# Kernel optimization log

Measured on AMD Instinct MI355X. Metric: run time of the kernel, lower is better.

The kernel has to match this reference:

```python
import jax, jax.numpy as jnp
import numpy as np

S, B, D, H = 2048, 2, 1024, 16
DK = D // H  # 64

def setup_inputs() -> dict:
    key0 = jax.random.key(0)
    ks = jax.random.split(key0, 11)
    scale = 0.02
    inp = {
        'query': jax.random.normal(ks[0], (S, B, D), jnp.float32),
        'key':   jax.random.normal(ks[1], (S, B, D), jnp.float32),
        'value': jax.random.normal(ks[2], (S, B, D), jnp.float32),
        # nn.Linear weights stored torch-style [out_features, in_features]
        'Wq': jax.random.normal(ks[3], (H * DK, D), jnp.float32) * scale,
        'bq': jnp.zeros((H * DK,), jnp.float32),
        'Wk': jax.random.normal(ks[4], (H * DK, D), jnp.float32) * scale,
        'bk': jnp.zeros((H * DK,), jnp.float32),
        'Wv': jax.random.normal(ks[5], (H * DK, D), jnp.float32) * scale,
        'bv': jnp.zeros((H * DK,), jnp.float32),
        'Wo': jax.random.normal(ks[6], (D, D), jnp.float32) * scale,
        'bo': jnp.zeros((D,), jnp.float32),
    }
    return inp

def _proj(x, W, b):
    # x: [S,B,D] -> [S,B,H,DK]
    y = jnp.einsum('sbd,ed->sbe', x, W) + b
    return y.reshape(x.shape[0], x.shape[1], H, DK)

def reference(query, key, value, Wq, bq, Wk, bk, Wv, bv, Wo, bo):
    q = _proj(query, Wq, bq)   # [S,B,H,DK]
    k = _proj(key,   Wk, bk)
    v = _proj(value, Wv, bv)
    # NOTE: original forward never applies self.scale -> unscaled QK^T (faithful)
    scores = jnp.einsum('ibhd,jbhd->ijbh', q, k)      # [Sq,Sk,B,H]
    attn = jax.nn.softmax(scores, axis=1)             # softmax over key axis j
    x = jnp.einsum('ijbh,jbhd->ibhd', attn, v)        # [S,B,H,DK]
    x = x.reshape(q.shape[0], q.shape[1], H * DK)     # [S,B,D]
    out = jnp.einsum('sbd,ed->sbe', x, Wo) + bo       # [S,B,D]
    return out
```

## Files before the change

### kernel.cpp

```cpp
#include <hip/hip_runtime.h>
#include <stdint.h>

#define S_LEN  2048
#define BATCH  2
#define DMODEL 1024
#define NHEAD  16
#define DKH    64

typedef __attribute__((ext_vector_type(8))) __bf16 bf16x8;
typedef __attribute__((ext_vector_type(4))) float  f32x4;
typedef unsigned short u16;
typedef unsigned int   u32;

#if __has_builtin(__builtin_amdgcn_exp2f)
#define EXP2(x) __builtin_amdgcn_exp2f(x)
#else
#define EXP2(x) __expf(0.69314718055994531f * (x))
#endif

__device__ __forceinline__ u16 f2bf(float f) {
  union { float f; u32 u; } v; v.f = f;
  u32 r = v.u + 0x7fffu + ((v.u >> 16) & 1u);
  return (u16)(r >> 16);
}

__global__ void cvt3_kernel(const float4* __restrict__ a, const float4* __restrict__ b,
                            const float4* __restrict__ c,
                            ushort4* __restrict__ oa, ushort4* __restrict__ ob,
                            ushort4* __restrict__ oc, int n4) {
  int i = blockIdx.x * blockDim.x + threadIdx.x;
  if (i >= n4) return;
  const float4* src = (blockIdx.y == 0) ? a : (blockIdx.y == 1) ? b : c;
  ushort4*      dst = (blockIdx.y == 0) ? oa : (blockIdx.y == 1) ? ob : oc;
  float4 v = src[i];
  ushort4 o;
  o.x = f2bf(v.x); o.y = f2bf(v.y); o.z = f2bf(v.z); o.w = f2bf(v.w);
  dst[i] = o;
}

__global__ void cvt4_kernel(const float4* __restrict__ a, const float4* __restrict__ b,
                            const float4* __restrict__ c, const float4* __restrict__ d,
                            ushort4* __restrict__ oa, ushort4* __restrict__ ob,
                            ushort4* __restrict__ oc, ushort4* __restrict__ od, int n4) {
  int i = blockIdx.x * blockDim.x + threadIdx.x;
  if (i >= n4) return;
  const float4* src = (blockIdx.y == 0) ? a : (blockIdx.y == 1) ? b : (blockIdx.y == 2) ? c : d;
  ushort4*      dst = (blockIdx.y == 0) ? oa : (blockIdx.y == 1) ? ob : (blockIdx.y == 2) ? oc : od;
  float4 v = src[i];
  ushort4 o;
  o.x = f2bf(v.x); o.y = f2bf(v.y); o.z = f2bf(v.z); o.w = f2bf(v.w);
  dst[i] = o;
}

__global__ __launch_bounds__(256, 2)
void gemm_qkv(const u16* __restrict__ Abase, const u16* __restrict__ Wbase,
              const float* __restrict__ b0, const float* __restrict__ b1,
              const float* __restrict__ b2, u16* __restrict__ Obase) {
  __shared__ __align__(16) u16 As[128 * 32];
  __shared__ __align__(16) u16 Bs[128 * 32];

  const int z = blockIdx.z;
  const u16* A = Abase + (size_t)z * (S_LEN * BATCH * DMODEL);
  const u16* W = Wbase + (size_t)z * (DMODEL * DMODEL);
  const float* bias = (z == 0) ? b0 : (z == 1) ? b1 : b2;
  u16* O = Obase + (size_t)z * (S_LEN * BATCH * DMODEL);
  const float scl = (z == 0) ? 1.4426950408889634f : 1.0f;

  const int tid  = threadIdx.x;
  const int wave = tid >> 6, lane = tid & 63;
  const int quad = lane >> 4, lcol = lane & 15;
  const int m0 = blockIdx.y * 128, n0 = blockIdx.x * 128;
  const int wm = (wave >> 1) * 64, wn = (wave & 1) * 64;

  f32x4 acc[4][4] = {};

  for (int k0 = 0; k0 < DMODEL; k0 += 32) {
#pragma unroll
    for (int r = 0; r < 2; ++r) {
      int idx = r * 256 + tid;
      int row = idx >> 2, col = (idx & 3) * 8;
      const u16* gA = A + (size_t)(m0 + row) * DMODEL + k0 + col;
      const u16* gW = W + (size_t)(n0 + row) * DMODEL + k0 + col;
      u16* lA = As + (size_t)(r * 256 + (tid & 192)) * 8;
      u16* lB = Bs + (size_t)(r * 256 + (tid & 192)) * 8;
      __builtin_amdgcn_global_load_lds((const __attribute__((address_space(1))) void*)gA,
                                       (__attribute__((address_space(3))) void*)lA, 16, 0, 0);
      __builtin_amdgcn_global_load_lds((const __attribute__((address_space(1))) void*)gW,
                                       (__attribute__((address_space(3))) void*)lB, 16, 0, 0);
    }
    __syncthreads();

    const u16* aBase = As + (wm + lcol) * 32 + quad * 8;
    const u16* bBase = Bs + (wn + lcol) * 32 + quad * 8;
    bf16x8 af[4], bfr[4];
#pragma unroll
    for (int i = 0; i < 4; ++i) af[i]  = *(const bf16x8*)(aBase + i * 16 * 32);
#pragma unroll
    for (int j = 0; j < 4; ++j) bfr[j] = *(const bf16x8*)(bBase + j * 16 * 32);
#pragma unroll
    for (int i = 0; i < 4; ++i)
#pragma unroll
      for (int j = 0; j < 4; ++j)
        acc[i][j] = __builtin_amdgcn_mfma_f32_16x16x32_bf16(af[i], bfr[j], acc[i][j], 0, 0, 0);
    __syncthreads();
  }

#pragma unroll
  for (int i = 0; i < 4; ++i) {
#pragma unroll
    for (int j = 0; j < 4; ++j) {
      int n = n0 + wn + j * 16 + lcol;
      int h = n >> 6, dk = n & 63;
      float bv = bias[n];
#pragma unroll
      for (int r = 0; r < 4; ++r) {
        int m = m0 + wm + i * 16 + quad * 4 + r;
        int s = m >> 1, b = m & 1;
        O[((size_t)(b * NHEAD + h) * S_LEN + s) * DKH + dk] = f2bf((acc[i][j][r] + bv) * scl);
      }
    }
  }
}

__global__ __launch_bounds__(256, 2)
void gemm_o(const u16* __restrict__ A, const u16* __restrict__ W,
            const float* __restrict__ bias, float* __restrict__ O) {
  __shared__ __align__(16) u16 As[128 * 32];
  __shared__ __align__(16) u16 Bs[64 * 32];

  const int tid  = threadIdx.x;
  const int wave = tid >> 6, lane = tid & 63;
  const int quad = lane >> 4, lcol = lane & 15;
  const int m0 = blockIdx.y * 128, n0 = blockIdx.x * 64;
  const int wm = (wave >> 1) * 64, wn = (wave & 1) * 32;

  f32x4 acc[4][2] = {};

  for (int k0 = 0; k0 < DMODEL; k0 += 32) {
#pragma unroll
    for (int r = 0; r < 2; ++r) {
      int idx = r * 256 + tid;
      int row = idx >> 2, col = (idx & 3) * 8;
      const u16* gA = A + (size_t)(m0 + row) * DMODEL + k0 + col;
      u16* lA = As + (size_t)(r * 256 + (tid & 192)) * 8;
      __builtin_amdgcn_global_load_lds((const __attribute__((address_space(1))) void*)gA,
                                       (__attribute__((address_space(3))) void*)lA, 16, 0, 0);
    }
    {
      int row = tid >> 2, col = (tid & 3) * 8;
      const u16* gW = W + (size_t)(n0 + row) * DMODEL + k0 + col;
      u16* lB = Bs + (size_t)(tid & 192) * 8;
      __builtin_amdgcn_global_load_lds((const __attribute__((address_space(1))) void*)gW,
                                       (__attribute__((address_space(3))) void*)lB, 16, 0, 0);
    }
    __syncthreads();

    const u16* aBase = As + (wm + lcol) * 32 + quad * 8;
    const u16* bBase = Bs + (wn + lcol) * 32 + quad * 8;
    bf16x8 af[4], bfr[2];
#pragma unroll
    for (int i = 0; i < 4; ++i) af[i]  = *(const bf16x8*)(aBase + i * 16 * 32);
#pragma unroll
    for (int j = 0; j < 2; ++j) bfr[j] = *(const bf16x8*)(bBase + j * 16 * 32);
#pragma unroll
    for (int i = 0; i < 4; ++i)
#pragma unroll
      for (int j = 0; j < 2; ++j)
        acc[i][j] = __builtin_amdgcn_mfma_f32_16x16x32_bf16(af[i], bfr[j], acc[i][j], 0, 0, 0);
    __syncthreads();
  }

#pragma unroll
  for (int i = 0; i < 4; ++i) {
#pragma unroll
    for (int j = 0; j < 2; ++j) {
      int n = n0 + wn + j * 16 + lcol;
      float bv = bias[n];
#pragma unroll
      for (int r = 0; r < 4; ++r) {
        int m = m0 + wm + i * 16 + quad * 4 + r;
        O[(size_t)m * DMODEL + n] = acc[i][j][r] + bv;
      }
    }
  }
}

__global__ __launch_bounds__(256, 2)
void attn_kernel(const u16* __restrict__ Q, const u16* __restrict__ K,
                 const u16* __restrict__ V, u16* __restrict__ O) {
  __shared__ __align__(16) u16 Ks[2][64 * 72];
  __shared__ __align__(16) u16 Vts[2][64 * 72];
  __shared__ __align__(16) u16 Ps[4][32 * 72];
  __shared__ float l_s[128];

  const int tid  = threadIdx.x;
  const int wave = tid >> 6, lane = tid & 63;
  const int quad = lane >> 4, lcol = lane & 15;
  const int bh = blockIdx.y;
  const int q0 = blockIdx.x * 128;

  const size_t headOff = (size_t)bh * S_LEN * DKH;
  const u16* Qg = Q + headOff;
  const u16* Kg = K + headOff;
  const u16* Vg = V + headOff;

  bf16x8 qf[2][2];
#pragma unroll
  for (int s = 0; s < 2; ++s)
#pragma unroll
    for (int ks = 0; ks < 2; ++ks)
      qf[s][ks] = *(const bf16x8*)(Qg + (size_t)(q0 + wave * 32 + s * 16 + lcol) * DKH +
                                   ks * 32 + quad * 8);

  const int vkp  = tid & 31;
  const int vo   = tid >> 5;
  const int krow = tid >> 3, kc0 = (tid & 7) * 8;

  {
    uint4 k0 = *(const uint4*)(Kg + (size_t)krow * DKH + kc0);
    uint4 k1 = *(const uint4*)(Kg + (size_t)(32 + krow) * DKH + kc0);
    const u16* vp = Vg + (size_t)(2 * vkp) * DKH + 8 * vo;
    uint4 a = *(const uint4*)vp;
    uint4 b = *(const uint4*)(vp + DKH);
    *(uint4*)(Ks[0] + krow * 72 + kc0)        = k0;
    *(uint4*)(Ks[0] + (32 + krow) * 72 + kc0) = k1;
#pragma unroll
    for (int w = 0; w < 4; ++w) {
      u32 aw = ((const u32*)&a)[w], bw = ((const u32*)&b)[w];
      *(u32*)(Vts[0] + (size_t)(8 * vo + 2 * w) * 72 + 2 * vkp)     = __builtin_amdgcn_perm(bw, aw, 0x05040100u);
      *(u32*)(Vts[0] + (size_t)(8 * vo + 2 * w + 1) * 72 + 2 * vkp) = __builtin_amdgcn_perm(bw, aw, 0x07060302u);
    }
  }

  f32x4 o_acc[2][4] = {};
  float lsum[2] = {0.f, 0.f};

  for (int it = 0; it < S_LEN / 64; ++it) {
    const int cur = it & 1;
    const int ktn = (it + 1) * 64;
    const bool has = (ktn < S_LEN);

    uint4 nk0, nk1, nva, nvb;
    if (has) {
      nk0 = *(const uint4*)(Kg + (size_t)(ktn + krow) * DKH + kc0);
      nk1 = *(const uint4*)(Kg + (size_t)(ktn + 32 + krow) * DKH + kc0);
      const u16* vp = Vg + (size_t)(ktn + 2 * vkp) * DKH + 8 * vo;
      nva = *(const uint4*)vp;
      nvb = *(const uint4*)(vp + DKH);
    }
    __syncthreads();

    const u16* ksrc = Ks[cur];
    const u16* vsrc = Vts[cur];

    f32x4 sc[2][4] = {};
#pragma unroll
    for (int ks = 0; ks < 2; ++ks) {
      bf16x8 ak[4];
#pragma unroll
      for (int j = 0; j < 4; ++j)
        ak[j] = *(const bf16x8*)(ksrc + (j * 16 + lcol) * 72 + ks * 32 + quad * 8);
      __builtin_amdgcn_s_setprio(1);
#pragma unroll
      for (int s = 0; s < 2; ++s)
#pragma unroll
        for (int j = 0; j < 4; ++j)
          sc[s][j] = __builtin_amdgcn_mfma_f32_16x16x32_bf16(ak[j], qf[s][ks], sc[s][j], 0, 0, 0);
      __builtin_amdgcn_s_setprio(0);
    }

#pragma unroll
    for (int s = 0; s < 2; ++s) {
      u16* prow = Ps[wave] + (s * 16 + lcol) * 72;
#pragma unroll
      for (int j = 0; j < 4; ++j) {
        float p0 = EXP2(sc[s][j][0]);
        float p1 = EXP2(sc[s][j][1]);
        float p2 = EXP2(sc[s][j][2]);
        float p3 = EXP2(sc[s][j][3]);
        lsum[s] += (p0 + p1) + (p2 + p3);
        u32 w0, w1;
        asm("v_cvt_pk_bf16_f32 %0, %1, %2" : "=v"(w0) : "v"(p0), "v"(p1));
        asm("v_cvt_pk_bf16_f32 %0, %1, %2" : "=v"(w1) : "v"(p2), "v"(p3));
        uint2 pk; pk.x = w0; pk.y = w1;
        *(uint2*)(prow + j * 16 + quad * 4) = pk;
      }
    }

#pragma unroll
    for (int ks = 0; ks < 2; ++ks) {
      bf16x8 bv[4];
#pragma unroll
      for (int jd = 0; jd < 4; ++jd)
        bv[jd] = *(const bf16x8*)(vsrc + (jd * 16 + lcol) * 72 + ks * 32 + quad * 8);
      __builtin_amdgcn_s_setprio(1);
#pragma unroll
      for (int s = 0; s < 2; ++s) {
        bf16x8 ap = *(const bf16x8*)(Ps[wave] + (s * 16 + lcol) * 72 + ks * 32 + quad * 8);
#pragma unroll
        for (int jd = 0; jd < 4; ++jd)
          o_acc[s][jd] = __builtin_amdgcn_mfma_f32_16x16x32_bf16(ap, bv[jd], o_acc[s][jd], 0, 0, 0);
      }
      __builtin_amdgcn_s_setprio(0);
    }

    if (has) {
      u16* kdst = Ks[cur ^ 1];
      u16* vdst = Vts[cur ^ 1];
      *(uint4*)(kdst + krow * 72 + kc0)        = nk0;
      *(uint4*)(kdst + (32 + krow) * 72 + kc0) = nk1;
#pragma unroll
      for (int w = 0; w < 4; ++w) {
        u32 aw = ((const u32*)&nva)[w], bw = ((const u32*)&nvb)[w];
        *(u32*)(vdst + (size_t)(8 * vo + 2 * w) * 72 + 2 * vkp)     = __builtin_amdgcn_perm(bw, aw, 0x05040100u);
        *(u32*)(vdst + (size_t)(8 * vo + 2 * w + 1) * 72 + 2 * vkp) = __builtin_amdgcn_perm(bw, aw, 0x07060302u);
      }
    }
  }

#pragma unroll
  for (int s = 0; s < 2; ++s) {
    lsum[s] += __shfl_xor(lsum[s], 16);
    lsum[s] += __shfl_xor(lsum[s], 32);
  }
  if (lane < 16) {
    l_s[wave * 32 + lane]      = lsum[0];
    l_s[wave * 32 + 16 + lane] = lsum[1];
  }
  __syncthreads();

  const int b = bh >> 4, h = bh & 15;
#pragma unroll
  for (int s = 0; s < 2; ++s) {
#pragma unroll
    for (int r = 0; r < 4; ++r) {
      float inv = 1.f / l_s[wave * 32 + s * 16 + quad * 4 + r];
      int sq = q0 + wave * 32 + s * 16 + quad * 4 + r;
#pragma unroll
      for (int jd = 0; jd < 4; ++jd) {
        int dk = jd * 16 + lcol;
        O[((size_t)(sq * BATCH + b)) * DMODEL + h * DKH + dk] = f2bf(o_acc[s][jd][r] * inv);
      }
    }
  }
}

extern "C" void kernel_launch(void* const* d_in, const int* in_sizes, int n_in,
                              void* d_out, int out_size, void* d_ws, size_t ws_size,
                              hipStream_t stream) {
  const float* q  = (const float*)d_in[0];
  const float* k  = (const float*)d_in[1];
  const float* v  = (const float*)d_in[2];
  const float* Wq = (const float*)d_in[3];
  const float* bq = (const float*)d_in[4];
  const float* Wk = (const float*)d_in[5];
  const float* bk = (const float*)d_in[6];
  const float* Wv = (const float*)d_in[7];
  const float* bv = (const float*)d_in[8];
  const float* Wo = (const float*)d_in[9];
  const float* bo = (const float*)d_in[10];

  const int NX = S_LEN * BATCH * DMODEL;
  const int NW = DMODEL * DMODEL;

  u16* ws  = (u16*)d_ws;
  u16* Xq  = ws;
  u16* Wqb = Xq  + 3 * (size_t)NX;
  u16* Qb  = Wqb + 4 * (size_t)NW;
  u16* Xo  = Qb  + 3 * (size_t)NX;

  u16* Xk  = Xq + NX, *Xv = Xq + 2 * (size_t)NX;
  u16* Wkb = Wqb + NW, *Wvb = Wqb + 2 * (size_t)NW, *Wob = Wqb + 3 * (size_t)NW;
  u16* Kb  = Qb + NX, *Vb = Qb + 2 * (size_t)NX;

  dim3 g3(NX / 4 / 256, 3);
  cvt3_kernel<<<g3, 256, 0, stream>>>((const float4*)q, (const float4*)k, (const float4*)v,
                                      (ushort4*)Xq, (ushort4*)Xk, (ushort4*)Xv, NX / 4);
  dim3 g4(NW / 4 / 256, 4);
  cvt4_kernel<<<g4, 256, 0, stream>>>((const float4*)Wq, (const float4*)Wk, (const float4*)Wv,
                                      (const float4*)Wo,
                                      (ushort4*)Wqb, (ushort4*)Wkb, (ushort4*)Wvb, (ushort4*)Wob,
                                      NW / 4);

  dim3 gqkv(DMODEL / 128, (S_LEN * BATCH) / 128, 3);
  gemm_qkv<<<gqkv, 256, 0, stream>>>(Xq, Wqb, bq, bk, bv, Qb);

  dim3 ga(S_LEN / 128, BATCH * NHEAD);
  attn_kernel<<<ga, 256, 0, stream>>>(Qb, Kb, Vb, Xo);

  dim3 go(DMODEL / 64, (S_LEN * BATCH) / 128);
  gemm_o<<<go, 256, 0, stream>>>(Xo, Wob, bo, (float*)d_out);
}
```

Measured before the change: 226.1 us.

## Use 8 waves per attention block with 16 query rows each

The attention kernel now launches 512 threads, giving each wave 16 query rows instead of 32. This halves per-wave accumulator and score registers and raises wave-level parallelism. K and V tile staging is split so half the waves load K and half load and transpose V. The row-sum exchange through shared memory and its extra barrier are replaced by a lane shuffle. In exchange, each K/V tile read from LDS is now shared across more waves, so LDS read traffic per MFMA doubles.

```diff
diff --git a/kernel.cpp b/kernel.cpp
--- a/kernel.cpp
+++ b/kernel.cpp
@@ -185,13 +185,12 @@
   }
 }
 
-__global__ __launch_bounds__(256, 2)
+__global__ __launch_bounds__(512, 4)
 void attn_kernel(const u16* __restrict__ Q, const u16* __restrict__ K,
                  const u16* __restrict__ V, u16* __restrict__ O) {
   __shared__ __align__(16) u16 Ks[2][64 * 72];
   __shared__ __align__(16) u16 Vts[2][64 * 72];
-  __shared__ __align__(16) u16 Ps[4][32 * 72];
-  __shared__ float l_s[128];
+  __shared__ __align__(16) u16 Ps[8][16 * 72];
 
   const int tid  = threadIdx.x;
   const int wave = tid >> 6, lane = tid & 63;
@@ -204,26 +203,26 @@
   const u16* Kg = K + headOff;
   const u16* Vg = V + headOff;
 
-  bf16x8 qf[2][2];
-#pragma unroll
-  for (int s = 0; s < 2; ++s)
-#pragma unroll
-    for (int ks = 0; ks < 2; ++ks)
-      qf[s][ks] = *(const bf16x8*)(Qg + (size_t)(q0 + wave * 32 + s * 16 + lcol) * DKH +
-                                   ks * 32 + quad * 8);
-
-  const int vkp  = tid & 31;
-  const int vo   = tid >> 5;
-  const int krow = tid >> 3, kc0 = (tid & 7) * 8;
-
-  {
+  bf16x8 qf[2];
+#pragma unroll
+  for (int ks = 0; ks < 2; ++ks)
+    qf[ks] = *(const bf16x8*)(Qg + (size_t)(q0 + wave * 16 + lcol) * DKH + ks * 32 + quad * 8);
+
+  const int t4   = tid & 255;
+  const int krow = t4 >> 3, kc0 = (t4 & 7) * 8;
+  const int vkp  = t4 & 31;
+  const int vo   = t4 >> 5;
+  const bool isK = (wave < 4);
+
+  if (isK) {
     uint4 k0 = *(const uint4*)(Kg + (size_t)krow * DKH + kc0);
     uint4 k1 = *(const uint4*)(Kg + (size_t)(32 + krow) * DKH + kc0);
+    *(uint4*)(Ks[0] + krow * 72 + kc0)        = k0;
+    *(uint4*)(Ks[0] + (32 + krow) * 72 + kc0) = k1;
+  } else {
     const u16* vp = Vg + (size_t)(2 * vkp) * DKH + 8 * vo;
     uint4 a = *(const uint4*)vp;
     uint4 b = *(const uint4*)(vp + DKH);
-    *(uint4*)(Ks[0] + krow * 72 + kc0)        = k0;
-    *(uint4*)(Ks[0] + (32 + krow) * 72 + kc0) = k1;
 #pragma unroll
     for (int w = 0; w < 4; ++w) {
       u32 aw = ((const u32*)&a)[w], bw = ((const u32*)&b)[w];
@@ -232,28 +231,31 @@
     }
   }
 
-  f32x4 o_acc[2][4] = {};
-  float lsum[2] = {0.f, 0.f};
+  f32x4 o_acc[4] = {};
+  float lsum = 0.f;
 
   for (int it = 0; it < S_LEN / 64; ++it) {
     const int cur = it & 1;
     const int ktn = (it + 1) * 64;
     const bool has = (ktn < S_LEN);
 
-    uint4 nk0, nk1, nva, nvb;
+    uint4 n0, n1;
     if (has) {
-      nk0 = *(const uint4*)(Kg + (size_t)(ktn + krow) * DKH + kc0);
-      nk1 = *(const uint4*)(Kg + (size_t)(ktn + 32 + krow) * DKH + kc0);
-      const u16* vp = Vg + (size_t)(ktn + 2 * vkp) * DKH + 8 * vo;
-      nva = *(const uint4*)vp;
-      nvb = *(const uint4*)(vp + DKH);
+      if (isK) {
+        n0 = *(const uint4*)(Kg + (size_t)(ktn + krow) * DKH + kc0);
+        n1 = *(const uint4*)(Kg + (size_t)(ktn + 32 + krow) * DKH + kc0);
+      } else {
+        const u16* vp = Vg + (size_t)(ktn + 2 * vkp) * DKH + 8 * vo;
+        n0 = *(const uint4*)vp;
+        n1 = *(const uint4*)(vp + DKH);
+      }
     }
     __syncthreads();
 
     const u16* ksrc = Ks[cur];
     const u16* vsrc = Vts[cur];
 
-    f32x4 sc[2][4] = {};
+    f32x4 sc[4] = {};
 #pragma unroll
     for (int ks = 0; ks < 2; ++ks) {
       bf16x8 ak[4];
@@ -262,23 +264,20 @@
         ak[j] = *(const bf16x8*)(ksrc + (j * 16 + lcol) * 72 + ks * 32 + quad * 8);
       __builtin_amdgcn_s_setprio(1);
 #pragma unroll
-      for (int s = 0; s < 2; ++s)
-#pragma unroll
-        for (int j = 0; j < 4; ++j)
-          sc[s][j] = __builtin_amdgcn_mfma_f32_16x16x32_bf16(ak[j], qf[s][ks], sc[s][j], 0, 0, 0);
+      for (int j = 0; j < 4; ++j)
+        sc[j] = __builtin_amdgcn_mfma_f32_16x16x32_bf16(ak[j], qf[ks], sc[j], 0, 0, 0);
       __builtin_amdgcn_s_setprio(0);
     }
 
-#pragma unroll
-    for (int s = 0; s < 2; ++s) {
-      u16* prow = Ps[wave] + (s * 16 + lcol) * 72;
+    {
+      u16* prow = Ps[wave] + lcol * 72;
 #pragma unroll
       for (int j = 0; j < 4; ++j) {
-        float p0 = EXP2(sc[s][j][0]);
-        float p1 = EXP2(sc[s][j][1]);
-        float p2 = EXP2(sc[s][j][2]);
-        float p3 = EXP2(sc[s][j][3]);
-        lsum[s] += (p0 + p1) + (p2 + p3);
+        float p0 = EXP2(sc[j][0]);
+        float p1 = EXP2(sc[j][1]);
+        float p2 = EXP2(sc[j][2]);
+        float p3 = EXP2(sc[j][3]);
+        lsum += (p0 + p1) + (p2 + p3);
         u32 w0, w1;
         asm("v_cvt_pk_bf16_f32 %0, %1, %2" : "=v"(w0) : "v"(p0), "v"(p1));
         asm("v_cvt_pk_bf16_f32 %0, %1, %2" : "=v"(w1) : "v"(p2), "v"(p3));
@@ -293,54 +292,43 @@
 #pragma unroll
       for (int jd = 0; jd < 4; ++jd)
         bv[jd] = *(const bf16x8*)(vsrc + (jd * 16 + lcol) * 72 + ks * 32 + quad * 8);
+      bf16x8 ap = *(const bf16x8*)(Ps[wave] + lcol * 72 + ks * 32 + quad * 8);
       __builtin_amdgcn_s_setprio(1);
 #pragma unroll
-      for (int s = 0; s < 2; ++s) {
-        bf16x8 ap = *(const bf16x8*)(Ps[wave] + (s * 16 + lcol) * 72 + ks * 32 + quad * 8);
-#pragma unroll
-        for (int jd = 0; jd < 4; ++jd)
-          o_acc[s][jd] = __builtin_amdgcn_mfma_f32_16x16x32_bf16(ap, bv[jd], o_acc[s][jd], 0, 0, 0);
-      }
+      for (int jd = 0; jd < 4; ++jd)
+        o_acc[jd] = __builtin_amdgcn_mfma_f32_16x16x32_bf16(ap, bv[jd], o_acc[jd], 0, 0, 0);
       __builtin_amdgcn_s_setprio(0);
     }
 
     if (has) {
-      u16* kdst = Ks[cur ^ 1];
-      u16* vdst = Vts[cur ^ 1];
-      *(uint4*)(kdst + krow * 72 + kc0)        = nk0;
-      *(uint4*)(kdst + (32 + krow) * 72 + kc0) = nk1;
-#pragma unroll
-      for (int w = 0; w < 4; ++w) {
-        u32 aw = ((const u32*)&nva)[w], bw = ((const u32*)&nvb)[w];
-        *(u32*)(vdst + (size_t)(8 * vo + 2 * w) * 72 + 2 * vkp)     = __builtin_amdgcn_perm(bw, aw, 0x05040100u);
-        *(u32*)(vdst + (size_t)(8 * vo + 2 * w + 1) * 72 + 2 * vkp) = __builtin_amdgcn_perm(bw, aw, 0x07060302u);
-      }
-    }
-  }
-
-#pragma unroll
-  for (int s = 0; s < 2; ++s) {
-    lsum[s] += __shfl_xor(lsum[s], 16);
-    lsum[s] += __shfl_xor(lsum[s], 32);
-  }
-  if (lane < 16) {
-    l_s[wave * 32 + lane]      = lsum[0];
-    l_s[wave * 32 + 16 + lane] = lsum[1];
-  }
-  __syncthreads();
+      if (isK) {
+        u16* kdst = Ks[cur ^ 1];
+        *(uint4*)(kdst + krow * 72 + kc0)        = n0;
+        *(uint4*)(kdst + (32 + krow) * 72 + kc0) = n1;
+      } else {
+        u16* vdst = Vts[cur ^ 1];
+#pragma unroll
+        for (int w = 0; w < 4; ++w) {
+          u32 aw = ((const u32*)&n0)[w], bw = ((const u32*)&n1)[w];
+          *(u32*)(vdst + (size_t)(8 * vo + 2 * w) * 72 + 2 * vkp)     = __builtin_amdgcn_perm(bw, aw, 0x05040100u);
+          *(u32*)(vdst + (size_t)(8 * vo + 2 * w + 1) * 72 + 2 * vkp) = __builtin_amdgcn_perm(bw, aw, 0x07060302u);
+        }
+      }
+    }
+  }
+
+  lsum += __shfl_xor(lsum, 16);
+  lsum += __shfl_xor(lsum, 32);
 
   const int b = bh >> 4, h = bh & 15;
 #pragma unroll
-  for (int s = 0; s < 2; ++s) {
-#pragma unroll
-    for (int r = 0; r < 4; ++r) {
-      float inv = 1.f / l_s[wave * 32 + s * 16 + quad * 4 + r];
-      int sq = q0 + wave * 32 + s * 16 + quad * 4 + r;
-#pragma unroll
-      for (int jd = 0; jd < 4; ++jd) {
-        int dk = jd * 16 + lcol;
-        O[((size_t)(sq * BATCH + b)) * DMODEL + h * DKH + dk] = f2bf(o_acc[s][jd][r] * inv);
-      }
+  for (int r = 0; r < 4; ++r) {
+    float inv = 1.f / __shfl(lsum, quad * 4 + r);
+    int sq = q0 + wave * 16 + quad * 4 + r;
+#pragma unroll
+    for (int jd = 0; jd < 4; ++jd) {
+      int dk = jd * 16 + lcol;
+      O[((size_t)(sq * BATCH + b)) * DMODEL + h * DKH + dk] = f2bf(o_acc[jd][r] * inv);
     }
   }
 }
@@ -386,7 +374,7 @@
   gemm_qkv<<<gqkv, 256, 0, stream>>>(Xq, Wqb, bq, bk, bv, Qb);
 
   dim3 ga(S_LEN / 128, BATCH * NHEAD);
-  attn_kernel<<<ga, 256, 0, stream>>>(Qb, Kb, Vb, Xo);
+  attn_kernel<<<ga, 512, 0, stream>>>(Qb, Kb, Vb, Xo);
 
   dim3 go(DMODEL / 64, (S_LEN * BATCH) / 128);
   gemm_o<<<go, 256, 0, stream>>>(Xo, Wob, bo, (float*)d_out);
```

Result: slower. 239.4 us (+5.9%).
